# Kernel tuning notes

Hardware: AMD Instinct MI355X
Metric: run time of the kernel (lower is better)

The kernel has to match this reference:

```python
import jax, jax.numpy as jnp
import numpy as np

N_NODES = 50000

def cheb_conv(x, edge_index, W, b):
    # PyG ChebConv, K=2, normalization='sym', lambda_max=2.0 (default):
    # scaled Laplacian L_hat = (2/lambda_max)*L - I = -D^{-1/2} A D^{-1/2} (zero diag).
    # Tx_0 = x, Tx_1 = L_hat @ x ; out = Tx_0 @ W[0] + Tx_1 @ W[1] + b
    src, dst = edge_index[0], edge_index[1]
    ones = jnp.ones(src.shape[0], x.dtype)
    deg = jax.ops.segment_sum(ones, src, num_segments=N_NODES)
    dinv = jnp.where(deg > 0, 1.0 / jnp.sqrt(deg), 0.0)
    norm = -dinv[src] * dinv[dst]                                   # [E]
    tx1 = jax.ops.segment_sum(x[src] * norm[:, None], dst, num_segments=N_NODES)
    return x @ W[0] + tx1 @ W[1] + b

def setup_inputs() -> dict:
    key = jax.random.key(0)
    ks = jax.random.split(key, 12)
    IN, OUT, E, P = 128, 2, 800000, 400000
    return {
        "x": jax.random.normal(ks[0], (N_NODES, IN), jnp.float32),
        "edge_index": jax.random.randint(ks[1], (2, E), 0, N_NODES),
        "E_pos": jax.random.randint(ks[2], (2, P), 0, N_NODES),
        "neg_edge_index": jax.random.randint(ks[3], (2, P), 0, N_NODES),
        "W1": jax.random.normal(ks[4], (2, IN, 300), jnp.float32) * 0.05,
        "b1": jnp.zeros((300,), jnp.float32),
        "W2": jax.random.normal(ks[5], (2, 300, 100), jnp.float32) * 0.05,
        "b2": jnp.zeros((100,), jnp.float32),
        "W3": jax.random.normal(ks[6], (2, 100, OUT), jnp.float32) * 0.05,
        "b3": jnp.zeros((OUT,), jnp.float32),
        "lin1_W": jax.random.normal(ks[7], (100, IN), jnp.float32) * 0.05,
        "lin1_b": jnp.zeros((100,), jnp.float32),
        "lin2_W": jax.random.normal(ks[8], (100, IN), jnp.float32) * 0.05,
        "lin2_b": jnp.zeros((100,), jnp.float32),
        "c1": jnp.full((1,), 0.5, jnp.float32),
        "c2": jnp.full((1,), 0.5, jnp.float32),
    }

def reference(x, edge_index, E_pos, neg_edge_index, W1, b1, W2, b2, W3, b3,
              lin1_W, lin1_b, lin2_W, lin2_b, c1, c2):
    # eval mode: F.dropout and dropout_edge are identity
    x0 = x
    h = jax.nn.relu(cheb_conv(x0, edge_index, W1, b1))
    x1 = jax.nn.relu(cheb_conv(h, edge_index, W2, b2))
    x2 = x1 + jax.nn.relu(x0 @ lin1_W.T + lin1_b)
    z = x1 + jax.nn.relu(x0 @ lin2_W.T + lin2_b)
    pos_score = jnp.sum(z[E_pos[0]] * z[E_pos[1]], axis=1)              # [P]
    pos_loss = -jnp.mean(jnp.log(jax.nn.sigmoid(pos_score) + 1e-15))
    neg_score = jnp.sum(z[neg_edge_index[0]] * z[neg_edge_index[1]], axis=1)
    neg_loss = -jnp.mean(jnp.log(1.0 - jax.nn.sigmoid(neg_score) + 1e-15))
    r_loss = pos_loss + neg_loss
    out = cheb_conv(x2, edge_index, W3, b3)                             # [N, out_channels]
    return (out, r_loss, c1, c2)
```

## Files before the change

kernel.cpp:

```cpp
#include <hip/hip_runtime.h>
#include <math.h>


typedef unsigned short ushort_t;
typedef unsigned char u8;
typedef __attribute__((ext_vector_type(8))) __bf16 bf16x8;
typedef __attribute__((ext_vector_type(8))) short s16x8;
typedef __attribute__((ext_vector_type(4))) float f32x4;
typedef __attribute__((ext_vector_type(2))) float f32x2;

#define NB_H 256
#define HW 12500
#define PW 25000

__device__ __forceinline__ f32x4 mfma16x16x32(s16x8 a, s16x8 b, f32x4 c) {
  return __builtin_amdgcn_mfma_f32_16x16x32_bf16(
      __builtin_bit_cast(bf16x8, a), __builtin_bit_cast(bf16x8, b), c, 0, 0, 0);
}
__device__ __forceinline__ ushort_t f2bf(float f) {
  union { float f; unsigned u; } c; c.f = f;
  unsigned r = (c.u + 0x7FFFu + ((c.u >> 16) & 1u)) >> 16;
  return (ushort_t)r;
}
__device__ __forceinline__ f32x2 cvt2lo(unsigned u) {
  return __builtin_amdgcn_cvt_pk_f32_fp8((int)u, false);
}
__device__ __forceinline__ f32x2 cvt2hi(unsigned u) {
  return __builtin_amdgcn_cvt_pk_f32_fp8((int)u, true);
}
__device__ __forceinline__ u8 f2fp8(float f) {
  return (u8)(__builtin_amdgcn_cvt_pk_fp8_f32(f, 0.f, 0, false) & 0xff);
}

template<int VAR, int NT, int KTOT>
__global__ __launch_bounds__(256) void gemm_mfma(
    const ushort_t* __restrict__ A0, const ushort_t* __restrict__ A1,
    const ushort_t* __restrict__ Wt,
    const float* __restrict__ bias0, const float* __restrict__ bias1,
    const float* __restrict__ x1,
    const float* __restrict__ W3c, const float* __restrict__ b3c,
    void* __restrict__ out0, void* __restrict__ out1,
    float* __restrict__ t0g, float* __restrict__ t1g, int M)
{
  constexpr int NF = NT / 32;
  __shared__ __align__(16) ushort_t As[64 * 40];
  __shared__ __align__(16) ushort_t Bs[NT * 40];
  __shared__ float w3s[400];
  const int tid  = threadIdx.x;
  const int lane = tid & 63, w = tid >> 6;
  const int m0 = blockIdx.x * 64;
  const int wm = (w & 1) * 32, wn = (w >> 1) * (NT / 2);
  if (VAR == 2) { for (int i = tid; i < 400; i += 256) w3s[i] = W3c[i]; }
  f32x4 acc[2][NF];
#pragma unroll
  for (int i = 0; i < 2; ++i)
#pragma unroll
    for (int j = 0; j < NF; ++j) acc[i][j] = (f32x4){0.f, 0.f, 0.f, 0.f};

  for (int k0 = 0; k0 < KTOT; k0 += 32) {
    {
      const int r = tid >> 2, c8 = (tid & 3) * 8;
      const int gm = m0 + r;
      uint4 v = {0u, 0u, 0u, 0u};
      if (gm < M) {
        if (VAR == 1) {
          const u8* s8 = (const u8*)A0 + (size_t)gm * 320 + k0 + c8;
          const uint2 r8 = *(const uint2*)s8;
          const f32x2 f0 = cvt2lo(r8.x), f1 = cvt2hi(r8.x);
          const f32x2 f2 = cvt2lo(r8.y), f3 = cvt2hi(r8.y);
          v.x = (unsigned)f2bf(f0.x) | ((unsigned)f2bf(f0.y) << 16);
          v.y = (unsigned)f2bf(f1.x) | ((unsigned)f2bf(f1.y) << 16);
          v.z = (unsigned)f2bf(f2.x) | ((unsigned)f2bf(f2.y) << 16);
          v.w = (unsigned)f2bf(f3.x) | ((unsigned)f2bf(f3.y) << 16);
        } else {
          const ushort_t* srcp;
          if (VAR == 0) srcp = (k0 < 128) ? A0 + (size_t)gm * 128 + k0 + c8
                                          : A1 + (size_t)gm * 128 + (k0 - 128) + c8;
          else srcp = A0 + (size_t)gm * 128 + k0 + c8;
          v = *(const uint4*)srcp;
        }
      }
      *(uint4*)&As[r * 40 + c8] = v;
    }
    {
      const int c8 = (tid & 3) * 8;
#pragma unroll
      for (int i = 0; i < (NT * 4 + 255) / 256; ++i) {
        const int r = (tid >> 2) + i * 64;
        if (r < NT)
          *(uint4*)&Bs[r * 40 + c8] = *(const uint4*)(Wt + (size_t)r * KTOT + k0 + c8);
      }
    }
    __syncthreads();
    s16x8 af[2], bfr[NF];
#pragma unroll
    for (int mi = 0; mi < 2; ++mi)
      af[mi] = *(const s16x8*)&As[(wm + mi * 16 + (lane & 15)) * 40 + (lane >> 4) * 8];
#pragma unroll
    for (int ni = 0; ni < NF; ++ni)
      bfr[ni] = *(const s16x8*)&Bs[(wn + ni * 16 + (lane & 15)) * 40 + (lane >> 4) * 8];
#pragma unroll
    for (int mi = 0; mi < 2; ++mi)
#pragma unroll
      for (int ni = 0; ni < NF; ++ni)
        acc[mi][ni] = mfma16x16x32(af[mi], bfr[ni], acc[mi][ni]);
    __syncthreads();
  }

  if (VAR == 2) {
#pragma unroll
    for (int mi = 0; mi < 2; ++mi)
#pragma unroll
      for (int r = 0; r < 4; ++r) {
        const int gRow = m0 + wm + mi * 16 + ((lane >> 4) << 2) + r;
        float p0 = 0.f, p1 = 0.f, p2 = 0.f, p3 = 0.f;
#pragma unroll
        for (int ni = 0; ni < NF; ++ni) {
          const int col = wn + ni * 16 + (lane & 15);
          const float v = acc[mi][ni][r];
          if (gRow < M) {
            if (col < 100) {
              const float x2v = x1[(size_t)gRow * 128 + col] + fmaxf(v + bias0[col], 0.f);
              p0 = fmaf(x2v, w3s[col * 2 + 0], p0);
              p1 = fmaf(x2v, w3s[col * 2 + 1], p1);
              p2 = fmaf(x2v, w3s[200 + col * 2 + 0], p2);
              p3 = fmaf(x2v, w3s[200 + col * 2 + 1], p3);
            } else if (col < 200) {
              const int c = col - 100;
              ((u8*)out1)[(size_t)gRow * 128 + c] =
                  f2fp8(x1[(size_t)gRow * 128 + c] + fmaxf(v + bias1[c], 0.f));
            }
          }
        }
        if (wn == 0) {
#pragma unroll
          for (int off = 8; off; off >>= 1) {
            p0 += __shfl_down(p0, off, 16);
            p1 += __shfl_down(p1, off, 16);
            p2 += __shfl_down(p2, off, 16);
            p3 += __shfl_down(p3, off, 16);
          }
          if ((lane & 15) == 0 && gRow < M) {
            t0g[(size_t)gRow * 2 + 0] = p0 + b3c[0];
            t0g[(size_t)gRow * 2 + 1] = p1 + b3c[1];
            t1g[(size_t)gRow * 2 + 0] = p2;
            t1g[(size_t)gRow * 2 + 1] = p3;
          }
        }
      }
  } else {
#pragma unroll
    for (int mi = 0; mi < 2; ++mi)
#pragma unroll
      for (int ni = 0; ni < NF; ++ni)
#pragma unroll
        for (int r = 0; r < 4; ++r) {
          const int gRow = m0 + wm + mi * 16 + ((lane >> 4) << 2) + r;
          const int col  = wn + ni * 16 + (lane & 15);
          if (gRow >= M) continue;
          const float v = acc[mi][ni][r];
          if (VAR == 0) {
            ((u8*)out0)[(size_t)gRow * 320 + col] =
                (col < 300) ? f2fp8(fmaxf(v + bias0[col], 0.f)) : (u8)0;
          } else {
            if (col < 100) ((float*)out0)[(size_t)gRow * 128 + col] = v + bias0[col];
            else if (col < 200) ((u8*)out1)[(size_t)gRow * 128 + (col - 100)] = f2fp8(v);
          }
        }
  }
}

__global__ void pack_cvt(const float* __restrict__ x, ushort_t* __restrict__ xb,
                         u8* __restrict__ xf8, int n4,
                         const float* __restrict__ W1, const float* __restrict__ W2,
                         const float* __restrict__ l1W, const float* __restrict__ l2W,
                         ushort_t* __restrict__ W1t, ushort_t* __restrict__ W2t,
                         ushort_t* __restrict__ Wlt) {
  const int i = blockIdx.x * 256 + threadIdx.x;
  if (i < n4) {
    const float4 v = ((const float4*)x)[i];
    ushort4 o; o.x = f2bf(v.x); o.y = f2bf(v.y); o.z = f2bf(v.z); o.w = f2bf(v.w);
    ((ushort4*)xb)[i] = o;
    int p = 0;
    p = __builtin_amdgcn_cvt_pk_fp8_f32(v.x, v.y, p, false);
    p = __builtin_amdgcn_cvt_pk_fp8_f32(v.z, v.w, p, true);
    ((unsigned*)xf8)[i] = (unsigned)p;
    return;
  }
  const int j = i - n4;
  if (j < 81920) {
    const int n = j >> 8, k = j & 255;
    float v = 0.f;
    if (n < 300) v = (k < 128) ? W1[k * 300 + n] : W1[38400 + (k - 128) * 300 + n];
    W1t[j] = f2bf(v);
  } else if (j < 153600) {
    const int jj = j - 81920;
    const int n = jj / 320, k = jj - n * 320;
    float v = 0.f;
    if (n < 200 && k < 300) v = W2[(n < 100 ? 0 : 30000) + k * 100 + (n % 100)];
    W2t[jj] = f2bf(v);
  } else if (j < 182272) {
    const int jj = j - 153600;
    const int n = jj >> 7, k = jj & 127;
    float v = 0.f;
    if (n < 100) v = l1W[n * 128 + k];
    else if (n < 200) v = l2W[(n - 100) * 128 + k];
    Wlt[jj] = f2bf(v);
  }
}

__global__ __launch_bounds__(256) void hist2(
    const int* __restrict__ src, const int* __restrict__ dst, int E, int M,
    unsigned* __restrict__ partS, unsigned* __restrict__ partD,
    ushort_t* __restrict__ rank)
{
  __shared__ unsigned hist[HW];
  const int b = blockIdx.x;
  const int cs = (E + NB_H - 1) / NB_H;
  const int e0 = b * cs;
  const int e1 = (e0 + cs < E) ? e0 + cs : E;
  for (int isD = 0; isD < 2; ++isD) {
    const int* keys = isD ? dst : src;
    unsigned* part = isD ? partD : partS;
    for (int r = 0; r < 2; ++r) {
      const int klo = r * 2 * HW;
      for (int i = threadIdx.x; i < HW; i += 256) hist[i] = 0;
      __syncthreads();
      for (int e = e0 + threadIdx.x; e < e1; e += 256) {
        const int k = keys[e] - klo;
        if ((unsigned)k < (unsigned)(2 * HW)) {
          const unsigned old = atomicAdd(&hist[k >> 1], (k & 1) ? 0x10000u : 1u);
          if (isD) rank[e] = (ushort_t)((old >> ((k & 1) * 16)) & 0xffffu);
        }
      }
      __syncthreads();
      for (int i = threadIdx.x; i < HW; i += 256)
        part[(size_t)b * PW + r * HW + i] = hist[i];
      __syncthreads();
    }
  }
}

__global__ __launch_bounds__(256) void reduce_base2(
    const unsigned* __restrict__ partS, unsigned* __restrict__ partD,
    float* __restrict__ dinv, int* __restrict__ cnt, int M)
{
  const int t = blockIdx.x * 256 + threadIdx.x;
  if (t < PW) {
    const int i = t;
    unsigned ssum = 0;
    for (int b = 0; b < NB_H; b += 8) {
      unsigned v[8];
#pragma unroll
      for (int q = 0; q < 8; ++q) v[q] = partS[(size_t)(b + q) * PW + i];
#pragma unroll
      for (int q = 0; q < 8; ++q) ssum += v[q];
    }
    const int k = 2 * i;
    const unsigned s0 = ssum & 0xffffu, s1 = ssum >> 16;
    if (k < M) dinv[k] = s0 ? 1.f / sqrtf((float)s0) : 0.f;
    if (k + 1 < M) dinv[k + 1] = s1 ? 1.f / sqrtf((float)s1) : 0.f;
  } else if (t < 2 * PW) {
    const int i = t - PW;
    unsigned run = 0;
    for (int b = 0; b < NB_H; b += 8) {
      unsigned v[8], pre[8];
#pragma unroll
      for (int q = 0; q < 8; ++q) v[q] = partD[(size_t)(b + q) * PW + i];
#pragma unroll
      for (int q = 0; q < 8; ++q) { pre[q] = run; run += v[q]; }
#pragma unroll
      for (int q = 0; q < 8; ++q) partD[(size_t)(b + q) * PW + i] = pre[q];
    }
    const int k = 2 * i;
    if (k < M) cnt[k] = (int)(run & 0xffffu);
    if (k + 1 < M) cnt[k + 1] = (int)(run >> 16);
  }
}

__global__ void scan_local(const int* __restrict__ cnt, int* __restrict__ ptr,
                           int* __restrict__ bsum, int n)
{
  __shared__ int tmp[256];
  const int i = blockIdx.x * 256 + threadIdx.x;
  const int v = (i < n) ? cnt[i] : 0;
  tmp[threadIdx.x] = v;
  __syncthreads();
  for (int off = 1; off < 256; off <<= 1) {
    const int t = (threadIdx.x >= off) ? tmp[threadIdx.x - off] : 0;
    __syncthreads();
    tmp[threadIdx.x] += t;
    __syncthreads();
  }
  if (i < n) ptr[i] = tmp[threadIdx.x] - v;
  if (threadIdx.x == 255) bsum[blockIdx.x] = tmp[255];
}
__global__ void scan_bsum(int* __restrict__ bsum, int nb, float* __restrict__ accs) {
  __shared__ int tmp[256];
  if (threadIdx.x < 2) accs[threadIdx.x] = 0.f;
  const int v = (threadIdx.x < nb) ? bsum[threadIdx.x] : 0;
  tmp[threadIdx.x] = v;
  __syncthreads();
  for (int off = 1; off < 256; off <<= 1) {
    const int t = (threadIdx.x >= off) ? tmp[threadIdx.x - off] : 0;
    __syncthreads();
    tmp[threadIdx.x] += t;
    __syncthreads();
  }
  if (threadIdx.x < nb) bsum[threadIdx.x] = tmp[threadIdx.x] - v;
}
__global__ void scan_add(int* __restrict__ ptr, const int* __restrict__ bsum, int n, int E) {
  const int i = blockIdx.x * 256 + threadIdx.x;
  if (i < n) ptr[i] += bsum[blockIdx.x];
  if (i == 0) ptr[n] = E;
}

__global__ void fill_csr2(const int* __restrict__ src, const int* __restrict__ dst,
                          const float* __restrict__ dinv, const int* __restrict__ ptr,
                          const unsigned* __restrict__ base32,
                          const ushort_t* __restrict__ rank,
                          int2* __restrict__ csr, int E)
{
  const int e = blockIdx.x * 256 + threadIdx.x;
  if (e >= E) return;
  const int cs = (E + NB_H - 1) / NB_H;
  const int b = e / cs;
  const int s = src[e], d = dst[e];
  const unsigned bv = base32[(size_t)b * PW + (d >> 1)];
  const int base = (int)((bv >> ((d & 1) * 16)) & 0xffffu);
  const int pos = ptr[d] + base + (int)rank[e];
  const float w = -dinv[s] * dinv[d];
  csr[pos] = make_int2(s, __float_as_int(w));
}

#define ACCV(u, ww) { f32x2 t; \
  t = cvt2lo(u.x); a[0]  = fmaf(ww, t.x, a[0]);  a[1]  = fmaf(ww, t.y, a[1]);  \
  t = cvt2hi(u.x); a[2]  = fmaf(ww, t.x, a[2]);  a[3]  = fmaf(ww, t.y, a[3]);  \
  t = cvt2lo(u.y); a[4]  = fmaf(ww, t.x, a[4]);  a[5]  = fmaf(ww, t.y, a[5]);  \
  t = cvt2hi(u.y); a[6]  = fmaf(ww, t.x, a[6]);  a[7]  = fmaf(ww, t.y, a[7]);  \
  t = cvt2lo(u.z); a[8]  = fmaf(ww, t.x, a[8]);  a[9]  = fmaf(ww, t.y, a[9]);  \
  t = cvt2hi(u.z); a[10] = fmaf(ww, t.x, a[10]); a[11] = fmaf(ww, t.y, a[11]); \
  t = cvt2lo(u.w); a[12] = fmaf(ww, t.x, a[12]); a[13] = fmaf(ww, t.y, a[13]); \
  t = cvt2hi(u.w); a[14] = fmaf(ww, t.x, a[14]); a[15] = fmaf(ww, t.y, a[15]); }

__global__ __launch_bounds__(256) void gather128e(
    const u8* __restrict__ xf8, ushort_t* __restrict__ txb,
    const int* __restrict__ ptr, const int2* __restrict__ csr, int M)
{
  const int node = (blockIdx.x * 256 + threadIdx.x) >> 3;
  const int sub  = threadIdx.x & 7;
  if (node >= M) return;
  const int beg = ptr[node], end = ptr[node + 1];
  float a[16] = {};
  int p = beg;
  for (; p + 8 <= end; p += 8) {
    int2 e[8];
#pragma unroll
    for (int q = 0; q < 8; ++q) e[q] = csr[p + q];
    uint4 v[8];
#pragma unroll
    for (int q = 0; q < 8; ++q)
      v[q] = *(const uint4*)(xf8 + (size_t)e[q].x * 128 + sub * 16);
#pragma unroll
    for (int q = 0; q < 8; ++q) { const float wq = __int_as_float(e[q].y); ACCV(v[q], wq) }
  }
  for (; p < end; ++p) {
    const int2 eq = csr[p]; const float wq = __int_as_float(eq.y);
    const uint4 v = *(const uint4*)(xf8 + (size_t)eq.x * 128 + sub * 16);
    ACCV(v, wq)
  }
  uint4 o1, o2;
  o1.x = (unsigned)f2bf(a[0])  | ((unsigned)f2bf(a[1])  << 16);
  o1.y = (unsigned)f2bf(a[2])  | ((unsigned)f2bf(a[3])  << 16);
  o1.z = (unsigned)f2bf(a[4])  | ((unsigned)f2bf(a[5])  << 16);
  o1.w = (unsigned)f2bf(a[6])  | ((unsigned)f2bf(a[7])  << 16);
  o2.x = (unsigned)f2bf(a[8])  | ((unsigned)f2bf(a[9])  << 16);
  o2.y = (unsigned)f2bf(a[10]) | ((unsigned)f2bf(a[11]) << 16);
  o2.z = (unsigned)f2bf(a[12]) | ((unsigned)f2bf(a[13]) << 16);
  o2.w = (unsigned)f2bf(a[14]) | ((unsigned)f2bf(a[15]) << 16);
  ushort_t* dstp = txb + (size_t)node * 128 + sub * 16;
  *(uint4*)dstp = o1;
  *(uint4*)(dstp + 8) = o2;
}

__global__ __launch_bounds__(256) void gather100e_x1(
    const u8* __restrict__ Brh, float* __restrict__ Ar,
    const int* __restrict__ ptr, const int2* __restrict__ csr, int M)
{
  const int node = (blockIdx.x * 256 + threadIdx.x) >> 3;
  const int sub  = threadIdx.x & 7;
  if (node >= M) return;
  const int beg = ptr[node], end = ptr[node + 1];
  float a[16] = {};
  int p = beg;
  for (; p + 8 <= end; p += 8) {
    int2 e[8];
#pragma unroll
    for (int q = 0; q < 8; ++q) e[q] = csr[p + q];
    uint4 v[8];
#pragma unroll
    for (int q = 0; q < 8; ++q)
      v[q] = *(const uint4*)(Brh + (size_t)e[q].x * 128 + sub * 16);
#pragma unroll
    for (int q = 0; q < 8; ++q) { const float wq = __int_as_float(e[q].y); ACCV(v[q], wq) }
  }
  for (; p < end; ++p) {
    const int2 eq = csr[p]; const float wq = __int_as_float(eq.y);
    const uint4 v = *(const uint4*)(Brh + (size_t)eq.x * 128 + sub * 16);
    ACCV(v, wq)
  }
  float* dstp = Ar + (size_t)node * 128 + sub * 16;
#pragma unroll
  for (int q = 0; q < 4; ++q) {
    float4 b = *(const float4*)(dstp + q * 4);
    b.x = fmaxf(b.x + a[q * 4 + 0], 0.f);
    b.y = fmaxf(b.y + a[q * 4 + 1], 0.f);
    b.z = fmaxf(b.z + a[q * 4 + 2], 0.f);
    b.w = fmaxf(b.w + a[q * 4 + 3], 0.f);
    *(float4*)(dstp + q * 4) = b;
  }
}
#undef ACCV

__device__ __forceinline__ void maskrow(uint4& r, int sub) {
  if (sub >= 6) { r.y = 0u; r.z = 0u; r.w = 0u; if (sub == 7) r.x = 0u; }
}
#define DOTV(uu, vv, s) { f32x2 p_, q_; \
  p_ = cvt2lo(uu.x); q_ = cvt2lo(vv.x); s = fmaf(p_.x, q_.x, s); s = fmaf(p_.y, q_.y, s); \
  p_ = cvt2hi(uu.x); q_ = cvt2hi(vv.x); s = fmaf(p_.x, q_.x, s); s = fmaf(p_.y, q_.y, s); \
  p_ = cvt2lo(uu.y); q_ = cvt2lo(vv.y); s = fmaf(p_.x, q_.x, s); s = fmaf(p_.y, q_.y, s); \
  p_ = cvt2hi(uu.y); q_ = cvt2hi(vv.y); s = fmaf(p_.x, q_.x, s); s = fmaf(p_.y, q_.y, s); \
  p_ = cvt2lo(uu.z); q_ = cvt2lo(vv.z); s = fmaf(p_.x, q_.x, s); s = fmaf(p_.y, q_.y, s); \
  p_ = cvt2hi(uu.z); q_ = cvt2hi(vv.z); s = fmaf(p_.x, q_.x, s); s = fmaf(p_.y, q_.y, s); \
  p_ = cvt2lo(uu.w); q_ = cvt2lo(vv.w); s = fmaf(p_.x, q_.x, s); s = fmaf(p_.y, q_.y, s); \
  p_ = cvt2hi(uu.w); q_ = cvt2hi(vv.w); s = fmaf(p_.x, q_.x, s); s = fmaf(p_.y, q_.y, s); }

__global__ __launch_bounds__(256) void loss_fp8(
    const u8* __restrict__ zf8, const int* __restrict__ ep,
    const int* __restrict__ en, int P, float* __restrict__ acc)
{
  __shared__ float red[8];
  const int tid = threadIdx.x;
  const int lane = tid & 63, wib = tid >> 6;
  const int sub = tid & 7;
  const int slot0 = blockIdx.x * 32 + (tid >> 3);
  const int step = gridDim.x * 32;
  float tp = 0.f, tn = 0.f;
  int g = slot0;
  for (; g + 3 * step < 2 * P; g += 4 * step) {
    int neg[4], na[4], nb[4];
#pragma unroll
    for (int q = 0; q < 4; ++q) {
      const int gq = g + q * step;
      neg[q] = (gq >= P);
      const int p = neg[q] ? gq - P : gq;
      const int* ia = neg[q] ? en : ep;
      na[q] = ia[p]; nb[q] = ia[P + p];
    }
    uint4 ra[4], rb[4];
#pragma unroll
    for (int q = 0; q < 4; ++q) {
      ra[q] = *(const uint4*)(zf8 + (size_t)na[q] * 128 + sub * 16);
      rb[q] = *(const uint4*)(zf8 + (size_t)nb[q] * 128 + sub * 16);
      maskrow(ra[q], sub); maskrow(rb[q], sub);
    }
    float s[4] = {0.f, 0.f, 0.f, 0.f};
#pragma unroll
    for (int q = 0; q < 4; ++q) DOTV(ra[q], rb[q], s[q])
#pragma unroll
    for (int off = 4; off; off >>= 1) {
#pragma unroll
      for (int q = 0; q < 4; ++q) s[q] += __shfl_down(s[q], off, 8);
    }
    if (sub == 0) {
#pragma unroll
      for (int q = 0; q < 4; ++q) {
        const float sig = 1.f / (1.f + expf(-s[q]));
        if (neg[q]) tn += logf(1.f - sig + 1e-15f); else tp += logf(sig + 1e-15f);
      }
    }
  }
  for (; g < 2 * P; g += step) {
    const int neg = (g >= P);
    const int p = neg ? g - P : g;
    const int* ia = neg ? en : ep;
    const int na = ia[p], nb = ia[P + p];
    uint4 ra = *(const uint4*)(zf8 + (size_t)na * 128 + sub * 16);
    uint4 rb = *(const uint4*)(zf8 + (size_t)nb * 128 + sub * 16);
    maskrow(ra, sub); maskrow(rb, sub);
    float s = 0.f;
    DOTV(ra, rb, s)
#pragma unroll
    for (int off = 4; off; off >>= 1) s += __shfl_down(s, off, 8);
    if (sub == 0) {
      const float sig = 1.f / (1.f + expf(-s));
      if (neg) tn += logf(1.f - sig + 1e-15f); else tp += logf(sig + 1e-15f);
    }
  }
  tp += __shfl_down(tp, 32, 64); tn += __shfl_down(tn, 32, 64);
  tp += __shfl_down(tp, 16, 64); tn += __shfl_down(tn, 16, 64);
  tp += __shfl_down(tp, 8, 64);  tn += __shfl_down(tn, 8, 64);
  if (lane == 0) { red[wib] = tp; red[4 + wib] = tn; }
  __syncthreads();
  if (tid == 0) {
    atomicAdd(acc + 0, red[0] + red[1] + red[2] + red[3]);
    atomicAdd(acc + 1, red[4] + red[5] + red[6] + red[7]);
  }
}
#undef DOTV

__global__ void gather2_final(
    const float* __restrict__ t1, const float* __restrict__ t0,
    const int* __restrict__ ptr, const int2* __restrict__ csr,
    const float* __restrict__ accs,
    const float* __restrict__ c1, const float* __restrict__ c2,
    float* __restrict__ out, int M, float invP)
{
  const int i = blockIdx.x * blockDim.x + threadIdx.x;
  if (i < M) {
    float a0 = 0.f, a1 = 0.f;
    const int beg = ptr[i], end = ptr[i + 1];
    int p = beg;
    for (; p + 4 <= end; p += 4) {
      const int2 e0 = csr[p], e1 = csr[p + 1], e2 = csr[p + 2], e3 = csr[p + 3];
      const float w0 = __int_as_float(e0.y), w1 = __int_as_float(e1.y);
      const float w2 = __int_as_float(e2.y), w3 = __int_as_float(e3.y);
      const float2 v0 = *(const float2*)(t1 + (size_t)e0.x * 2);
      const float2 v1 = *(const float2*)(t1 + (size_t)e1.x * 2);
      const float2 v2 = *(const float2*)(t1 + (size_t)e2.x * 2);
      const float2 v3 = *(const float2*)(t1 + (size_t)e3.x * 2);
      a0 = fmaf(w0, v0.x, a0); a1 = fmaf(w0, v0.y, a1);
      a0 = fmaf(w1, v1.x, a0); a1 = fmaf(w1, v1.y, a1);
      a0 = fmaf(w2, v2.x, a0); a1 = fmaf(w2, v2.y, a1);
      a0 = fmaf(w3, v3.x, a0); a1 = fmaf(w3, v3.y, a1);
    }
    for (; p < end; ++p) {
      const int2 eq = csr[p]; const float wq = __int_as_float(eq.y);
      const float2 v = *(const float2*)(t1 + (size_t)eq.x * 2);
      a0 = fmaf(wq, v.x, a0); a1 = fmaf(wq, v.y, a1);
    }
    const float2 base = *(const float2*)(t0 + (size_t)i * 2);
    *(float2*)(out + (size_t)i * 2) = make_float2(base.x + a0, base.y + a1);
  }
  if (i == 0) {
    out[2 * M + 0] = -(accs[0] + accs[1]) * invP;
    out[2 * M + 1] = c1[0];
    out[2 * M + 2] = c2[0];
  }
}

extern "C" void kernel_launch(void* const* d_in, const int* in_sizes, int n_in,
                              void* d_out, int out_size, void* d_ws, size_t ws_size,
                              hipStream_t stream)
{
  const float* x   = (const float*)d_in[0];
  const int*   ei  = (const int*)d_in[1];
  const int*   ep  = (const int*)d_in[2];
  const int*   en  = (const int*)d_in[3];
  const float* W1  = (const float*)d_in[4];
  const float* b1  = (const float*)d_in[5];
  const float* W2  = (const float*)d_in[6];
  const float* b2  = (const float*)d_in[7];
  const float* W3  = (const float*)d_in[8];
  const float* b3  = (const float*)d_in[9];
  const float* l1W = (const float*)d_in[10];
  const float* l1b = (const float*)d_in[11];
  const float* l2W = (const float*)d_in[12];
  const float* l2b = (const float*)d_in[13];
  const float* c1  = (const float*)d_in[14];
  const float* c2  = (const float*)d_in[15];
  float* out = (float*)d_out;

  const int M = in_sizes[0] / 128;
  const int E = in_sizes[1] / 2;
  const int P = in_sizes[2] / 2;
  const int* src = ei;
  const int* dst = ei + E;
  const int nb_scan = (M + 255) / 256;

  float* ws = (float*)d_ws;
  size_t o = 0;
  float*    dinv = ws + o;            o += 50176;
  int*      cnt  = (int*)(ws + o);    o += (size_t)M;
  int*      ptr  = (int*)(ws + o);    o += (size_t)M + 8;
  int*      bsum = (int*)(ws + o);    o += 256;
  int2*     csr  = (int2*)(ws + o);   o += (size_t)E * 2;
  ushort_t* rank = (ushort_t*)(ws + o); o += (size_t)E / 2;
  ushort_t* xb   = (ushort_t*)(ws + o); o += (size_t)M * 64;
  u8*       xf8  = (u8*)(ws + o);     o += (size_t)M * 32;
  ushort_t* tx0b = (ushort_t*)(ws + o); o += (size_t)M * 64;
  ushort_t* W1t  = (ushort_t*)(ws + o); o += 40960;
  ushort_t* W2t  = (ushort_t*)(ws + o); o += 35840;
  ushort_t* Wlt  = (ushort_t*)(ws + o); o += 14336;
  u8*       h8   = (u8*)(ws + o);     o += (size_t)M * 160;
  float*    Ar   = ws + o;            o += (size_t)M * 128;
  u8*       Brh  = (u8*)(ws + o);     o += (size_t)M * 32;
  u8*       zf8  = (u8*)(ws + o);     o += (size_t)M * 32;
  float*    t0   = ws + o;            o += (size_t)M * 2;
  float*    t1   = ws + o;            o += (size_t)M * 2;
  float*    accs = ws + o;            o += 8;
  unsigned* partS = (unsigned*)h8;
  unsigned* partD = (unsigned*)Ar;

  const int n4 = M * 32;
  pack_cvt<<<(n4 + 182272 + 255) / 256, 256, 0, stream>>>(
      x, xb, xf8, n4, W1, W2, l1W, l2W, W1t, W2t, Wlt);

  hist2<<<NB_H, 256, 0, stream>>>(src, dst, E, M, partS, partD, rank);
  reduce_base2<<<(2 * PW + 255) / 256, 256, 0, stream>>>(partS, partD, dinv, cnt, M);
  scan_local<<<nb_scan, 256, 0, stream>>>(cnt, ptr, bsum, M);
  scan_bsum<<<1, 256, 0, stream>>>(bsum, nb_scan, accs);
  scan_add<<<nb_scan, 256, 0, stream>>>(ptr, bsum, M, E);
  fill_csr2<<<(E + 255) / 256, 256, 0, stream>>>(src, dst, dinv, ptr, partD, rank, csr, E);

  const int gB = (M + 63) / 64;
  const int gE8 = (M * 8 + 255) / 256;

  gather128e<<<gE8, 256, 0, stream>>>(xf8, tx0b, ptr, csr, M);
  gemm_mfma<0, 320, 256><<<gB, 256, 0, stream>>>(
      xb, tx0b, W1t, b1, nullptr, nullptr, nullptr, nullptr, h8, nullptr, nullptr, nullptr, M);

  gemm_mfma<1, 224, 320><<<gB, 256, 0, stream>>>(
      (const ushort_t*)h8, nullptr, W2t, b2, nullptr, nullptr, nullptr, nullptr,
      Ar, Brh, nullptr, nullptr, M);
  gather100e_x1<<<gE8, 256, 0, stream>>>(Brh, Ar, ptr, csr, M);

  gemm_mfma<2, 224, 128><<<gB, 256, 0, stream>>>(
      xb, nullptr, Wlt, l1b, l2b, Ar , W3, b3, nullptr, zf8, t0, t1, M);

  loss_fp8<<<2048, 256, 0, stream>>>(zf8, ep, en, P, accs);

  gather2_final<<<(M + 255) / 256, 256, 0, stream>>>(t1, t0, ptr, csr,
                                                     accs, c1, c2, out, M, 1.0f / (float)P);
}
```

Baseline: 471.4 us.

## Merge independent kernels to cut launch count and overlap work

Folds the edge histogram into the pack/convert kernel as extra blocks, and splits the src and dst histograms across separate blocks so they run in parallel. Merges the block-sum scan with the scan-add step, with each block recomputing the small prefix itself. Runs the link-prediction loss and the final 2-column gather as disjoint block ranges of one launch, and moves the scalar outputs into a tiny trailing kernel. The aim is fewer launches and more overlap of independent work, at the cost of redundant prefix computation per block and an extra tiny launch.

```diff
diff --git a/kernel.cpp b/kernel.cpp
--- a/kernel.cpp
+++ b/kernel.cpp
@@ -12,6 +12,7 @@
 #define NB_H 256
 #define HW 12500
 #define PW 25000
+#define LOSS_NB 2048
 
 __device__ __forceinline__ f32x4 mfma16x16x32(s16x8 a, s16x8 b, f32x4 c) {
   return __builtin_amdgcn_mfma_f32_16x16x32_bf16(
@@ -170,13 +171,46 @@
   }
 }
 
-__global__ void pack_cvt(const float* __restrict__ x, ushort_t* __restrict__ xb,
-                         u8* __restrict__ xf8, int n4,
-                         const float* __restrict__ W1, const float* __restrict__ W2,
-                         const float* __restrict__ l1W, const float* __restrict__ l2W,
-                         ushort_t* __restrict__ W1t, ushort_t* __restrict__ W2t,
-                         ushort_t* __restrict__ Wlt) {
-  const int i = blockIdx.x * 256 + threadIdx.x;
+__global__ __launch_bounds__(256) void prep(
+    const int* __restrict__ src, const int* __restrict__ dst, int E, int M,
+    unsigned* __restrict__ partS, unsigned* __restrict__ partD,
+    ushort_t* __restrict__ rank,
+    const float* __restrict__ x, ushort_t* __restrict__ xb,
+    u8* __restrict__ xf8, int n4,
+    const float* __restrict__ W1, const float* __restrict__ W2,
+    const float* __restrict__ l1W, const float* __restrict__ l2W,
+    ushort_t* __restrict__ W1t, ushort_t* __restrict__ W2t,
+    ushort_t* __restrict__ Wlt)
+{
+  __shared__ unsigned hist[HW];
+  const int blk = blockIdx.x;
+  if (blk < 512) {
+    const int isD = (blk >= 256);
+    const int b = isD ? blk - 256 : blk;
+    const int* keys = isD ? dst : src;
+    unsigned* part = isD ? partD : partS;
+    const int cs = (E + NB_H - 1) / NB_H;
+    const int e0 = b * cs;
+    const int e1 = (e0 + cs < E) ? e0 + cs : E;
+    for (int r = 0; r < 2; ++r) {
+      const int klo = r * 2 * HW;
+      for (int i = threadIdx.x; i < HW; i += 256) hist[i] = 0;
+      __syncthreads();
+      for (int e = e0 + threadIdx.x; e < e1; e += 256) {
+        const int k = keys[e] - klo;
+        if ((unsigned)k < (unsigned)(2 * HW)) {
+          const unsigned old = atomicAdd(&hist[k >> 1], (k & 1) ? 0x10000u : 1u);
+          if (isD) rank[e] = (ushort_t)((old >> ((k & 1) * 16)) & 0xffffu);
+        }
+      }
+      __syncthreads();
+      for (int i = threadIdx.x; i < HW; i += 256)
+        part[(size_t)b * PW + r * HW + i] = hist[i];
+      __syncthreads();
+    }
+    return;
+  }
+  const int i = (blk - 512) * 256 + threadIdx.x;
   if (i < n4) {
     const float4 v = ((const float4*)x)[i];
     ushort4 o; o.x = f2bf(v.x); o.y = f2bf(v.y); o.z = f2bf(v.z); o.w = f2bf(v.w);
@@ -209,38 +243,6 @@
   }
 }
 
-__global__ __launch_bounds__(256) void hist2(
-    const int* __restrict__ src, const int* __restrict__ dst, int E, int M,
-    unsigned* __restrict__ partS, unsigned* __restrict__ partD,
-    ushort_t* __restrict__ rank)
-{
-  __shared__ unsigned hist[HW];
-  const int b = blockIdx.x;
-  const int cs = (E + NB_H - 1) / NB_H;
-  const int e0 = b * cs;
-  const int e1 = (e0 + cs < E) ? e0 + cs : E;
-  for (int isD = 0; isD < 2; ++isD) {
-    const int* keys = isD ? dst : src;
-    unsigned* part = isD ? partD : partS;
-    for (int r = 0; r < 2; ++r) {
-      const int klo = r * 2 * HW;
-      for (int i = threadIdx.x; i < HW; i += 256) hist[i] = 0;
-      __syncthreads();
-      for (int e = e0 + threadIdx.x; e < e1; e += 256) {
-        const int k = keys[e] - klo;
-        if ((unsigned)k < (unsigned)(2 * HW)) {
-          const unsigned old = atomicAdd(&hist[k >> 1], (k & 1) ? 0x10000u : 1u);
-          if (isD) rank[e] = (ushort_t)((old >> ((k & 1) * 16)) & 0xffffu);
-        }
-      }
-      __syncthreads();
-      for (int i = threadIdx.x; i < HW; i += 256)
-        part[(size_t)b * PW + r * HW + i] = hist[i];
-      __syncthreads();
-    }
-  }
-}
-
 __global__ __launch_bounds__(256) void reduce_base2(
     const unsigned* __restrict__ partS, unsigned* __restrict__ partD,
     float* __restrict__ dinv, int* __restrict__ cnt, int M)
@@ -295,9 +297,10 @@
   if (i < n) ptr[i] = tmp[threadIdx.x] - v;
   if (threadIdx.x == 255) bsum[blockIdx.x] = tmp[255];
 }
-__global__ void scan_bsum(int* __restrict__ bsum, int nb, float* __restrict__ accs) {
+__global__ void scan_add2(int* __restrict__ ptr, const int* __restrict__ bsum,
+                          int n, int E, int nb, float* __restrict__ accs)
+{
   __shared__ int tmp[256];
-  if (threadIdx.x < 2) accs[threadIdx.x] = 0.f;
   const int v = (threadIdx.x < nb) ? bsum[threadIdx.x] : 0;
   tmp[threadIdx.x] = v;
   __syncthreads();
@@ -307,12 +310,11 @@
     tmp[threadIdx.x] += t;
     __syncthreads();
   }
-  if (threadIdx.x < nb) bsum[threadIdx.x] = tmp[threadIdx.x] - v;
-}
-__global__ void scan_add(int* __restrict__ ptr, const int* __restrict__ bsum, int n, int E) {
+  __syncthreads();
+  const int offset = (blockIdx.x > 0) ? tmp[blockIdx.x - 1] : 0;
   const int i = blockIdx.x * 256 + threadIdx.x;
-  if (i < n) ptr[i] += bsum[blockIdx.x];
-  if (i == 0) ptr[n] = E;
+  if (i < n) ptr[i] += offset;
+  if (i == 0) { ptr[n] = E; accs[0] = 0.f; accs[1] = 0.f; }
 }
 
 __global__ void fill_csr2(const int* __restrict__ src, const int* __restrict__ dst,
@@ -435,89 +437,17 @@
   p_ = cvt2lo(uu.w); q_ = cvt2lo(vv.w); s = fmaf(p_.x, q_.x, s); s = fmaf(p_.y, q_.y, s); \
   p_ = cvt2hi(uu.w); q_ = cvt2hi(vv.w); s = fmaf(p_.x, q_.x, s); s = fmaf(p_.y, q_.y, s); }
 
-__global__ __launch_bounds__(256) void loss_fp8(
+__global__ __launch_bounds__(256) void loss_g2(
     const u8* __restrict__ zf8, const int* __restrict__ ep,
-    const int* __restrict__ en, int P, float* __restrict__ acc)
-{
-  __shared__ float red[8];
-  const int tid = threadIdx.x;
-  const int lane = tid & 63, wib = tid >> 6;
-  const int sub = tid & 7;
-  const int slot0 = blockIdx.x * 32 + (tid >> 3);
-  const int step = gridDim.x * 32;
-  float tp = 0.f, tn = 0.f;
-  int g = slot0;
-  for (; g + 3 * step < 2 * P; g += 4 * step) {
-    int neg[4], na[4], nb[4];
-#pragma unroll
-    for (int q = 0; q < 4; ++q) {
-      const int gq = g + q * step;
-      neg[q] = (gq >= P);
-      const int p = neg[q] ? gq - P : gq;
-      const int* ia = neg[q] ? en : ep;
-      na[q] = ia[p]; nb[q] = ia[P + p];
-    }
-    uint4 ra[4], rb[4];
-#pragma unroll
-    for (int q = 0; q < 4; ++q) {
-      ra[q] = *(const uint4*)(zf8 + (size_t)na[q] * 128 + sub * 16);
-      rb[q] = *(const uint4*)(zf8 + (size_t)nb[q] * 128 + sub * 16);
-      maskrow(ra[q], sub); maskrow(rb[q], sub);
-    }
-    float s[4] = {0.f, 0.f, 0.f, 0.f};
-#pragma unroll
-    for (int q = 0; q < 4; ++q) DOTV(ra[q], rb[q], s[q])
-#pragma unroll
-    for (int off = 4; off; off >>= 1) {
-#pragma unroll
-      for (int q = 0; q < 4; ++q) s[q] += __shfl_down(s[q], off, 8);
-    }
-    if (sub == 0) {
-#pragma unroll
-      for (int q = 0; q < 4; ++q) {
-        const float sig = 1.f / (1.f + expf(-s[q]));
-        if (neg[q]) tn += logf(1.f - sig + 1e-15f); else tp += logf(sig + 1e-15f);
-      }
-    }
-  }
-  for (; g < 2 * P; g += step) {
-    const int neg = (g >= P);
-    const int p = neg ? g - P : g;
-    const int* ia = neg ? en : ep;
-    const int na = ia[p], nb = ia[P + p];
-    uint4 ra = *(const uint4*)(zf8 + (size_t)na * 128 + sub * 16);
-    uint4 rb = *(const uint4*)(zf8 + (size_t)nb * 128 + sub * 16);
-    maskrow(ra, sub); maskrow(rb, sub);
-    float s = 0.f;
-    DOTV(ra, rb, s)
-#pragma unroll
-    for (int off = 4; off; off >>= 1) s += __shfl_down(s, off, 8);
-    if (sub == 0) {
-      const float sig = 1.f / (1.f + expf(-s));
-      if (neg) tn += logf(1.f - sig + 1e-15f); else tp += logf(sig + 1e-15f);
-    }
-  }
-  tp += __shfl_down(tp, 32, 64); tn += __shfl_down(tn, 32, 64);
-  tp += __shfl_down(tp, 16, 64); tn += __shfl_down(tn, 16, 64);
-  tp += __shfl_down(tp, 8, 64);  tn += __shfl_down(tn, 8, 64);
-  if (lane == 0) { red[wib] = tp; red[4 + wib] = tn; }
-  __syncthreads();
-  if (tid == 0) {
-    atomicAdd(acc + 0, red[0] + red[1] + red[2] + red[3]);
-    atomicAdd(acc + 1, red[4] + red[5] + red[6] + red[7]);
-  }
-}
-#undef DOTV
-
-__global__ void gather2_final(
+    const int* __restrict__ en, int P, float* __restrict__ acc,
     const float* __restrict__ t1, const float* __restrict__ t0,
     const int* __restrict__ ptr, const int2* __restrict__ csr,
-    const float* __restrict__ accs,
-    const float* __restrict__ c1, const float* __restrict__ c2,
-    float* __restrict__ out, int M, float invP)
-{
-  const int i = blockIdx.x * blockDim.x + threadIdx.x;
-  if (i < M) {
+    float* __restrict__ out, int M)
+{
+  const int tid = threadIdx.x;
+  if (blockIdx.x >= LOSS_NB) {
+    const int i = (blockIdx.x - LOSS_NB) * 256 + tid;
+    if (i >= M) return;
     float a0 = 0.f, a1 = 0.f;
     const int beg = ptr[i], end = ptr[i + 1];
     int p = beg;
@@ -541,12 +471,84 @@
     }
     const float2 base = *(const float2*)(t0 + (size_t)i * 2);
     *(float2*)(out + (size_t)i * 2) = make_float2(base.x + a0, base.y + a1);
-  }
-  if (i == 0) {
-    out[2 * M + 0] = -(accs[0] + accs[1]) * invP;
-    out[2 * M + 1] = c1[0];
-    out[2 * M + 2] = c2[0];
-  }
+    return;
+  }
+  __shared__ float red[8];
+  const int lane = tid & 63, wib = tid >> 6;
+  const int sub = tid & 7;
+  const int slot0 = blockIdx.x * 32 + (tid >> 3);
+  const int step = LOSS_NB * 32;
+  float tp = 0.f, tn = 0.f;
+  int g = slot0;
+  for (; g + 3 * step < 2 * P; g += 4 * step) {
+    int neg[4], na[4], nb[4];
+#pragma unroll
+    for (int q = 0; q < 4; ++q) {
+      const int gq = g + q * step;
+      neg[q] = (gq >= P);
+      const int p = neg[q] ? gq - P : gq;
+      const int* ia = neg[q] ? en : ep;
+      na[q] = ia[p]; nb[q] = ia[P + p];
+    }
+    uint4 ra[4], rb[4];
+#pragma unroll
+    for (int q = 0; q < 4; ++q) {
+      ra[q] = *(const uint4*)(zf8 + (size_t)na[q] * 128 + sub * 16);
+      rb[q] = *(const uint4*)(zf8 + (size_t)nb[q] * 128 + sub * 16);
+      maskrow(ra[q], sub); maskrow(rb[q], sub);
+    }
+    float s[4] = {0.f, 0.f, 0.f, 0.f};
+#pragma unroll
+    for (int q = 0; q < 4; ++q) DOTV(ra[q], rb[q], s[q])
+#pragma unroll
+    for (int off = 4; off; off >>= 1) {
+#pragma unroll
+      for (int q = 0; q < 4; ++q) s[q] += __shfl_down(s[q], off, 8);
+    }
+    if (sub == 0) {
+#pragma unroll
+      for (int q = 0; q < 4; ++q) {
+        const float sig = 1.f / (1.f + expf(-s[q]));
+        if (neg[q]) tn += logf(1.f - sig + 1e-15f); else tp += logf(sig + 1e-15f);
+      }
+    }
+  }
+  for (; g < 2 * P; g += step) {
+    const int neg = (g >= P);
+    const int p = neg ? g - P : g;
+    const int* ia = neg ? en : ep;
+    const int na = ia[p], nb = ia[P + p];
+    uint4 ra = *(const uint4*)(zf8 + (size_t)na * 128 + sub * 16);
+    uint4 rb = *(const uint4*)(zf8 + (size_t)nb * 128 + sub * 16);
+    maskrow(ra, sub); maskrow(rb, sub);
+    float s = 0.f;
+    DOTV(ra, rb, s)
+#pragma unroll
+    for (int off = 4; off; off >>= 1) s += __shfl_down(s, off, 8);
+    if (sub == 0) {
+      const float sig = 1.f / (1.f + expf(-s));
+      if (neg) tn += logf(1.f - sig + 1e-15f); else tp += logf(sig + 1e-15f);
+    }
+  }
+  tp += __shfl_down(tp, 32, 64); tn += __shfl_down(tn, 32, 64);
+  tp += __shfl_down(tp, 16, 64); tn += __shfl_down(tn, 16, 64);
+  tp += __shfl_down(tp, 8, 64);  tn += __shfl_down(tn, 8, 64);
+  if (lane == 0) { red[wib] = tp; red[4 + wib] = tn; }
+  __syncthreads();
+  if (tid == 0) {
+    atomicAdd(acc + 0, red[0] + red[1] + red[2] + red[3]);
+    atomicAdd(acc + 1, red[4] + red[5] + red[6] + red[7]);
+  }
+}
+#undef DOTV
+
+__global__ void final_scalars(const float* __restrict__ accs,
+                              const float* __restrict__ c1, const float* __restrict__ c2,
+                              float* __restrict__ out, int M, float invP)
+{
+  out[2 * M + 0] = -(accs[0] + accs[1]) * invP;
+  out[2 * M + 1] = c1[0];
+  out[2 * M + 2] = c2[0];
 }
 
 extern "C" void kernel_launch(void* const* d_in, const int* in_sizes, int n_in,
@@ -603,14 +605,14 @@
   unsigned* partD = (unsigned*)Ar;
 
   const int n4 = M * 32;
-  pack_cvt<<<(n4 + 182272 + 255) / 256, 256, 0, stream>>>(
+  const int packBlocks = (n4 + 182272 + 255) / 256;
+  prep<<<512 + packBlocks, 256, 0, stream>>>(
+      src, dst, E, M, partS, partD, rank,
       x, xb, xf8, n4, W1, W2, l1W, l2W, W1t, W2t, Wlt);
 
-  hist2<<<NB_H, 256, 0, stream>>>(src, dst, E, M, partS, partD, rank);
   reduce_base2<<<(2 * PW + 255) / 256, 256, 0, stream>>>(partS, partD, dinv, cnt, M);
   scan_local<<<nb_scan, 256, 0, stream>>>(cnt, ptr, bsum, M);
-  scan_bsum<<<1, 256, 0, stream>>>(bsum, nb_scan, accs);
-  scan_add<<<nb_scan, 256, 0, stream>>>(ptr, bsum, M, E);
+  scan_add2<<<nb_scan, 256, 0, stream>>>(ptr, bsum, M, E, nb_scan, accs);
   fill_csr2<<<(E + 255) / 256, 256, 0, stream>>>(src, dst, dinv, ptr, partD, rank, csr, E);
 
   const int gB = (M + 63) / 64;
@@ -628,8 +630,7 @@
   gemm_mfma<2, 224, 128><<<gB, 256, 0, stream>>>(
       xb, nullptr, Wlt, l1b, l2b, Ar , W3, b3, nullptr, zf8, t0, t1, M);
 
-  loss_fp8<<<2048, 256, 0, stream>>>(zf8, ep, en, P, accs);
-
-  gather2_final<<<(M + 255) / 256, 256, 0, stream>>>(t1, t0, ptr, csr,
-                                                     accs, c1, c2, out, M, 1.0f / (float)P);
-}
+  loss_g2<<<LOSS_NB + nb_scan, 256, 0, stream>>>(
+      zf8, ep, en, P, accs, t1, t0, ptr, csr, out, M);
+  final_scalars<<<1, 1, 0, stream>>>(accs, c1, c2, out, M, 1.0f / (float)P);
+}
```

Result: no change. 465.6 us (-1.2%).
